# Optimization experiments

Measured on AMD Instinct MI355X. Metric: run time of the kernel, lower is better.

Reference implementation:

```python
import jax, jax.numpy as jnp
import numpy as np

D_MODEL = 2048
D_FFN = 8192
RANK = 16
MOD_SCALE = 0.1
EPS = 1e-6


def setup_inputs() -> dict:
    key = jax.random.key(0)
    ks = jax.random.split(key, 8)
    B, S = 2, 2048
    init_scale = 0.01
    return {
        'hidden_states': jax.random.normal(ks[0], (B, S, D_MODEL), jnp.float32),
        'attn_output': jax.random.normal(ks[1], (B, S, D_MODEL), jnp.float32),
        'A': jax.random.normal(ks[2], (D_MODEL, RANK), jnp.float32) * (init_scale / np.sqrt(D_MODEL)),
        'Bmat': jax.random.normal(ks[3], (RANK, D_FFN), jnp.float32) * (init_scale / np.sqrt(RANK)),
        'W_in': jax.random.normal(ks[4], (D_FFN, D_MODEL), jnp.float32) * 0.02,  # gate_proj.weight
        'W_up': jax.random.normal(ks[5], (D_FFN, D_MODEL), jnp.float32) * 0.02,  # up_proj.weight
        'W_down': jax.random.normal(ks[6], (D_MODEL, D_FFN), jnp.float32) * 0.02,  # down_proj.weight
        'gamma': jnp.ones((D_MODEL,), jnp.float32),  # post_attention_layernorm (RMSNorm) weight
    }


def _rmsnorm(x, gamma):
    var = jnp.mean(x * x, axis=-1, keepdims=True)
    return x * jax.lax.rsqrt(var + EPS) * gamma


def reference(hidden_states, attn_output, A, Bmat, W_in, W_up, W_down, gamma):
    residual = hidden_states
    # Neuro-plastic modulation: [B,S,r]
    modulation = MOD_SCALE * jnp.tanh(jnp.einsum('bsd,dr->bsr', attn_output, A))
    # NPT applies post-attn norm to the residual (not residual+attn)
    h = _rmsnorm(residual, gamma)  # [B,S,d_model]
    # Fused per-token weight delta: delta_w^T @ h == B^T ((A^T h) * mod)
    hA = jnp.einsum('bsd,dr->bsr', h, A)  # [B,S,r]
    delta_out = jnp.einsum('bsr,rf->bsf', hA * modulation, Bmat)  # [B,S,d_ffn]
    gate = jax.nn.silu(jnp.einsum('bsd,fd->bsf', h, W_in) + delta_out)
    up = jnp.einsum('bsd,fd->bsf', h, W_up)
    out = jnp.einsum('bsf,df->bsd', gate * up, W_down)
    return residual + out
```

## Files before the change

kernel.cpp:

```cpp
#include <hip/hip_runtime.h>
#include <cstdint>
#include <cstddef>

#define D_MODEL 2048
#define D_FFN   8192
#define RANK    16
#define EPS     1e-6f
#define MOD_SCALE 0.1f

typedef float    f32x4 __attribute__((ext_vector_type(4)));
typedef _Float16 half8 __attribute__((ext_vector_type(8)));

__device__ __forceinline__ void async_load16(const void* g, void* l) {
  __builtin_amdgcn_global_load_lds(
      (const __attribute__((address_space(1))) uint32_t*)g,
      (__attribute__((address_space(3))) uint32_t*)l,
      16, 0, 0);
}

__device__ __forceinline__ void stage_round(const _Float16* __restrict__ g,
                                            size_t stride, _Float16* l, int tid) {
  const int row = tid >> 3;
  const int cs  = (tid & 7) ^ (row & 7);
  async_load16(g + (size_t)row * stride + (size_t)cs * 8, l + tid * 8);
}

__device__ __forceinline__ half8 frag64(const _Float16* base, int row, int ck) {
  return *(const half8*)&base[row * 64 + ((ck ^ (row & 7)) * 8)];
}

#define PRIO1() __builtin_amdgcn_s_setprio(1)
#define PRIO0() __builtin_amdgcn_s_setprio(0)
#define VMW(n)  asm volatile("s_waitcnt vmcnt(" #n ")" ::: "memory")
#define BARM()  asm volatile("s_barrier" ::: "memory")

__global__ __launch_bounds__(256) void convert3_f32_f16(
    const float* __restrict__ s0, const float* __restrict__ s1,
    const float* __restrict__ s2,
    _Float16* __restrict__ d0, _Float16* __restrict__ d1,
    _Float16* __restrict__ d2)
{
  const int w = blockIdx.x >> 13;
  const float*   s = (w == 0) ? s0 : (w == 1) ? s1 : s2;
  _Float16*      d = (w == 0) ? d0 : (w == 1) ? d1 : d2;
  size_t i = ((size_t)(blockIdx.x & 8191) * 256 + threadIdx.x) * 8;
  f32x4 a = *(const f32x4*)(s + i);
  f32x4 b = *(const f32x4*)(s + i + 4);
  half8 h;
  #pragma unroll
  for (int j = 0; j < 4; ++j) { h[j] = (_Float16)a[j]; h[4+j] = (_Float16)b[j]; }
  *(half8*)(d + i) = h;
}

__global__ __launch_bounds__(256) void convert_f32_f16(
    const float* __restrict__ s, _Float16* __restrict__ d)
{
  size_t i = ((size_t)blockIdx.x * 256 + threadIdx.x) * 8;
  f32x4 a = *(const f32x4*)(s + i);
  f32x4 b = *(const f32x4*)(s + i + 4);
  half8 h;
  #pragma unroll
  for (int j = 0; j < 4; ++j) { h[j] = (_Float16)a[j]; h[4+j] = (_Float16)b[j]; }
  *(half8*)(d + i) = h;
}

__global__ __launch_bounds__(256) void prep_kernel(
    const float* __restrict__ hs, const float* __restrict__ attn,
    const float* __restrict__ Amat, const float* __restrict__ gamma,
    _Float16* __restrict__ h16, float* __restrict__ cmat)
{
  const int token = blockIdx.x;
  const int tid   = threadIdx.x;
  const int lane  = tid & 63;
  const int wv    = tid >> 6;
  const size_t tb = (size_t)token * D_MODEL;
  const int base  = tid * 8;

  f32x4 x0 = *(const f32x4*)(hs + tb + base);
  f32x4 x1 = *(const f32x4*)(hs + tb + base + 4);
  f32x4 a0 = *(const f32x4*)(attn + tb + base);
  f32x4 a1 = *(const f32x4*)(attn + tb + base + 4);

  float ss = 0.f;
  #pragma unroll
  for (int j = 0; j < 4; ++j) ss += x0[j]*x0[j] + x1[j]*x1[j];
  #pragma unroll
  for (int off = 32; off > 0; off >>= 1) ss += __shfl_xor(ss, off, 64);

  __shared__ float red[4];
  __shared__ float redp[4][RANK];
  __shared__ float redh[4][RANK];
  if (lane == 0) red[wv] = ss;
  __syncthreads();
  const float tot = red[0] + red[1] + red[2] + red[3];
  const float rms = rsqrtf(tot * (1.0f / D_MODEL) + EPS);

  f32x4 g0 = *(const f32x4*)(gamma + base);
  f32x4 g1 = *(const f32x4*)(gamma + base + 4);
  float hv[8], av[8];
  #pragma unroll
  for (int j = 0; j < 4; ++j) {
    hv[j]   = x0[j] * rms * g0[j];
    hv[4+j] = x1[j] * rms * g1[j];
    av[j]   = a0[j];
    av[4+j] = a1[j];
  }
  half8 hh;
  #pragma unroll
  for (int j = 0; j < 8; ++j) hh[j] = (_Float16)hv[j];
  *(half8*)(h16 + tb + base) = hh;

  float pa[RANK], ph[RANK];
  #pragma unroll
  for (int r = 0; r < RANK; ++r) { pa[r] = 0.f; ph[r] = 0.f; }
  #pragma unroll
  for (int e = 0; e < 8; ++e) {
    const f32x4* Ar = (const f32x4*)(Amat + (size_t)(base + e) * RANK);
    #pragma unroll
    for (int q = 0; q < 4; ++q) {
      f32x4 ar = Ar[q];
      #pragma unroll
      for (int j = 0; j < 4; ++j) {
        pa[q*4+j] += av[e] * ar[j];
        ph[q*4+j] += hv[e] * ar[j];
      }
    }
  }
  #pragma unroll
  for (int r = 0; r < RANK; ++r) {
    #pragma unroll
    for (int off = 32; off > 0; off >>= 1) {
      pa[r] += __shfl_xor(pa[r], off, 64);
      ph[r] += __shfl_xor(ph[r], off, 64);
    }
  }
  if (lane == 0) {
    #pragma unroll
    for (int r = 0; r < RANK; ++r) { redp[wv][r] = pa[r]; redh[wv][r] = ph[r]; }
  }
  __syncthreads();
  if (tid < RANK) {
    float sp = redp[0][tid] + redp[1][tid] + redp[2][tid] + redp[3][tid];
    float sh = redh[0][tid] + redh[1][tid] + redh[2][tid] + redh[3][tid];
    cmat[(size_t)token * RANK + tid] = sh * (MOD_SCALE * tanhf(sp));
  }
}

#define BGOFF 16384
#define BUOFF 24576

__global__ __launch_bounds__(512, 2) void gemm_gateup(
    const _Float16* __restrict__ h16,
    const _Float16* __restrict__ Wg16, const _Float16* __restrict__ Wu16,
    const float* __restrict__ cmat, const float* __restrict__ Bmat,
    _Float16* __restrict__ tmat)
{
  __shared__ __align__(16) _Float16 lds[2][32768];

  const int tid  = threadIdx.x;
  const int lane = tid & 63;
  const int wv   = tid >> 6;
  const int lr   = lane & 15;
  const int quad = lane >> 4;
  const int qb   = (wv >> 2) * 2;
  const int e    = wv & 3;
  const int wm   = (wv >> 2) * 128;

  const int lin  = blockIdx.x;
  const int xcd  = lin & 7;
  const int r    = lin >> 3;
  const int gm0  = (xcd * 2 + (r & 1)) * 256;
  const int gn0  = (r >> 1) * 128;

  constexpr int NT = D_MODEL / 64;

  f32x4 accG[8][2], accU[8][2];
  #pragma unroll
  for (int i = 0; i < 8; ++i)
    #pragma unroll
    for (int j = 0; j < 2; ++j) {
      f32x4 z = {0.f, 0.f, 0.f, 0.f};
      accG[i][j] = z; accU[i][j] = z;
    }

#define STA(b,q,t)  stage_round(h16  + (size_t)(gm0 + (q)*64) * D_MODEL + (size_t)(t)*64, D_MODEL, &lds[b][(q)*4096], tid)
#define STBG(b,p,t) stage_round(Wg16 + (size_t)(gn0 + (p)*64) * D_MODEL + (size_t)(t)*64, D_MODEL, &lds[b][BGOFF + (p)*4096], tid)
#define STBU(b,p,t) stage_round(Wu16 + (size_t)(gn0 + (p)*64) * D_MODEL + (size_t)(t)*64, D_MODEL, &lds[b][BUOFF + (p)*4096], tid)
#define STAGE_ALL(b,t) do { STA(b,0,t); STA(b,1,t); STA(b,2,t); STA(b,3,t); \
                            STBG(b,0,t); STBG(b,1,t); STBU(b,0,t); STBU(b,1,t); } while (0)

  STAGE_ALL(0, 0);
  VMW(0); BARM();

  for (int t = 0; t < NT; ++t) {
    const int cur = t & 1, nxt = cur ^ 1;
    const _Float16* A   = &lds[cur][0];
    const _Float16* Bgp = &lds[cur][BGOFF + e * 2048];
    const _Float16* Bup = &lds[cur][BUOFF + e * 2048];

    if (t + 1 < NT) STAGE_ALL(nxt, t + 1);

    half8 bg[2][2], bu[2][2], af[4][2];
    #pragma unroll
    for (int inn = 0; inn < 2; ++inn)
      #pragma unroll
      for (int kk = 0; kk < 2; ++kk) {
        bg[inn][kk] = frag64(Bgp, inn*16 + lr, kk*4 + quad);
        bu[inn][kk] = frag64(Bup, inn*16 + lr, kk*4 + quad);
      }
    #pragma unroll
    for (int im = 0; im < 4; ++im)
      #pragma unroll
      for (int kk = 0; kk < 2; ++kk)
        af[im][kk] = frag64(A + (qb + 0) * 4096, im*16 + lr, kk*4 + quad);

    PRIO1();
    #pragma unroll
    for (int im = 0; im < 4; ++im)
      #pragma unroll
      for (int inn = 0; inn < 2; ++inn)
        #pragma unroll
        for (int kk = 0; kk < 2; ++kk) {
          accG[im][inn] = __builtin_amdgcn_mfma_f32_16x16x32_f16(af[im][kk], bg[inn][kk], accG[im][inn], 0, 0, 0);
          accU[im][inn] = __builtin_amdgcn_mfma_f32_16x16x32_f16(af[im][kk], bu[inn][kk], accU[im][inn], 0, 0, 0);
        }
    PRIO0();

    half8 ao[4][2];
    #pragma unroll
    for (int im = 0; im < 4; ++im)
      #pragma unroll
      for (int kk = 0; kk < 2; ++kk)
        ao[im][kk] = frag64(A + (qb + 1) * 4096, im*16 + lr, kk*4 + quad);

    PRIO1();
    #pragma unroll
    for (int im = 0; im < 4; ++im)
      #pragma unroll
      for (int inn = 0; inn < 2; ++inn)
        #pragma unroll
        for (int kk = 0; kk < 2; ++kk) {
          accG[4+im][inn] = __builtin_amdgcn_mfma_f32_16x16x32_f16(ao[im][kk], bg[inn][kk], accG[4+im][inn], 0, 0, 0);
          accU[4+im][inn] = __builtin_amdgcn_mfma_f32_16x16x32_f16(ao[im][kk], bu[inn][kk], accU[4+im][inn], 0, 0, 0);
        }
    PRIO0();

    VMW(0); BARM();
  }

  __syncthreads();
  _Float16* l0 = &lds[0][0];
  for (int i = tid; i < 8192; i += 512) {
    int m = i >> 5, k = i & 31;
    l0[i] = (k < RANK) ? (_Float16)cmat[(size_t)(gm0 + m) * RANK + k] : (_Float16)0.f;
  }
  for (int i = tid; i < 4096; i += 512) {
    int f = i >> 5, k = i & 31;
    l0[8192 + i] = (k < RANK) ? (_Float16)Bmat[(size_t)k * D_FFN + gn0 + f] : (_Float16)0.f;
  }
  __syncthreads();
  #pragma unroll
  for (int ai = 0; ai < 8; ++ai) {
    half8 cf = *(const half8*)&l0[(wm + ai*16 + lr) * 32 + quad * 8];
    #pragma unroll
    for (int inn = 0; inn < 2; ++inn) {
      half8 bd = *(const half8*)&l0[8192 + (e*32 + inn*16 + lr) * 32 + quad * 8];
      accG[ai][inn] = __builtin_amdgcn_mfma_f32_16x16x32_f16(cf, bd, accG[ai][inn], 0, 0, 0);
    }
  }

  #pragma unroll
  for (int ai = 0; ai < 8; ++ai)
    #pragma unroll
    for (int inn = 0; inn < 2; ++inn) {
      const int grow = gm0 + wm + ai*16 + quad*4;
      const int gcol = gn0 + e*32 + inn*16 + lr;
      #pragma unroll
      for (int rr = 0; rr < 4; ++rr) {
        float g = accG[ai][inn][rr];
        float u = accU[ai][inn][rr];
        float s = g / (1.0f + __expf(-g));
        tmat[(size_t)(grow + rr) * D_FFN + gcol] = (_Float16)(s * u);
      }
    }
#undef STA
#undef STBG
#undef STBU
#undef STAGE_ALL
}

__global__ __launch_bounds__(512, 2) void gemm_down(
    const _Float16* __restrict__ tmat, const _Float16* __restrict__ Wd16,
    const float* __restrict__ hs, float* __restrict__ out)
{
  __shared__ __align__(16) _Float16 lds[3][24576];

  const int tid  = threadIdx.x;
  const int lane = tid & 63;
  const int wv   = tid >> 6;
  const int lr   = lane & 15;
  const int quad = lane >> 4;
  const int qb   = (wv >> 2) * 2;
  const int e    = wv & 3;
  const int wm   = (wv >> 2) * 128;

  const int lin  = blockIdx.x;
  const int xcd  = lin & 7;
  const int r    = lin >> 3;
  const int gn0  = (xcd * 2 + (r & 1)) * 128;
  const int gm0  = (r >> 1) * 256;

  constexpr int NT = D_FFN / 64;

  f32x4 acc[8][2];
  #pragma unroll
  for (int i = 0; i < 8; ++i)
    #pragma unroll
    for (int j = 0; j < 2; ++j) {
      f32x4 z = {0.f, 0.f, 0.f, 0.f};
      acc[i][j] = z;
    }

#define DSTA(b,q,t) stage_round(tmat + (size_t)(gm0 + (q)*64) * D_FFN + (size_t)(t)*64, D_FFN, &lds[b][(q)*4096], tid)
#define DSTB(b,p,t) stage_round(Wd16 + (size_t)(gn0 + (p)*64) * D_FFN + (size_t)(t)*64, D_FFN, &lds[b][16384 + (p)*4096], tid)
#define DSTAGE_ALL(b,t) do { DSTA(b,0,t); DSTA(b,1,t); DSTA(b,2,t); DSTA(b,3,t); \
                             DSTB(b,0,t); DSTB(b,1,t); } while (0)

  DSTAGE_ALL(0, 0);
  DSTAGE_ALL(1, 1);
  VMW(6); BARM();

  int cur = 0;
  for (int t = 0; t < NT; ++t) {
    const _Float16* A = &lds[cur][0];
    const _Float16* B = &lds[cur][16384 + e * 2048];
    int nx2 = cur + 2; if (nx2 >= 3) nx2 -= 3;

    if (t + 2 < NT) DSTAGE_ALL(nx2, t + 2);

    half8 bf[2][2], af[4][2];
    #pragma unroll
    for (int inn = 0; inn < 2; ++inn)
      #pragma unroll
      for (int kk = 0; kk < 2; ++kk)
        bf[inn][kk] = frag64(B, inn*16 + lr, kk*4 + quad);
    #pragma unroll
    for (int im = 0; im < 4; ++im)
      #pragma unroll
      for (int kk = 0; kk < 2; ++kk)
        af[im][kk] = frag64(A + (qb + 0) * 4096, im*16 + lr, kk*4 + quad);

    PRIO1();
    #pragma unroll
    for (int im = 0; im < 4; ++im)
      #pragma unroll
      for (int inn = 0; inn < 2; ++inn)
        #pragma unroll
        for (int kk = 0; kk < 2; ++kk)
          acc[im][inn] = __builtin_amdgcn_mfma_f32_16x16x32_f16(af[im][kk], bf[inn][kk], acc[im][inn], 0, 0, 0);
    PRIO0();

    half8 ao[4][2];
    #pragma unroll
    for (int im = 0; im < 4; ++im)
      #pragma unroll
      for (int kk = 0; kk < 2; ++kk)
        ao[im][kk] = frag64(A + (qb + 1) * 4096, im*16 + lr, kk*4 + quad);

    PRIO1();
    #pragma unroll
    for (int im = 0; im < 4; ++im)
      #pragma unroll
      for (int inn = 0; inn < 2; ++inn)
        #pragma unroll
        for (int kk = 0; kk < 2; ++kk)
          acc[4+im][inn] = __builtin_amdgcn_mfma_f32_16x16x32_f16(ao[im][kk], bf[inn][kk], acc[4+im][inn], 0, 0, 0);
    PRIO0();

    if (t + 2 < NT) { VMW(6); } else { VMW(0); }
    BARM();

    cur += 1; if (cur >= 3) cur -= 3;
  }

  #pragma unroll
  for (int ai = 0; ai < 8; ++ai)
    #pragma unroll
    for (int inn = 0; inn < 2; ++inn) {
      const int grow = gm0 + wm + ai*16 + quad*4;
      const int gcol = gn0 + e*32 + inn*16 + lr;
      #pragma unroll
      for (int rr = 0; rr < 4; ++rr) {
        size_t o = (size_t)(grow + rr) * D_MODEL + gcol;
        out[o] = hs[o] + acc[ai][inn][rr];
      }
    }
#undef DSTA
#undef DSTB
#undef DSTAGE_ALL
}

extern "C" void kernel_launch(void* const* d_in, const int* in_sizes, int n_in,
                              void* d_out, int out_size, void* d_ws, size_t ws_size,
                              hipStream_t stream) {
  const float* hs    = (const float*)d_in[0];
  const float* attn  = (const float*)d_in[1];
  const float* Amat  = (const float*)d_in[2];
  const float* Bmat  = (const float*)d_in[3];
  const float* Wg    = (const float*)d_in[4];
  const float* Wu    = (const float*)d_in[5];
  const float* Wd    = (const float*)d_in[6];
  const float* gamma = (const float*)d_in[7];
  float* out = (float*)d_out;

  const int M = in_sizes[0] / D_MODEL;
  const size_t WD = (size_t)D_FFN * D_MODEL;

  char* ws = (char*)d_ws;
  _Float16* h16  = (_Float16*)ws;
  float*    cmat = (float*)(ws + (size_t)M * D_MODEL * 2);
  _Float16* tmat = (_Float16*)(ws + (size_t)M * D_MODEL * 2 + (size_t)M * RANK * 4);
  _Float16* wbuf = tmat + (size_t)M * D_FFN;
  _Float16* Wg16 = wbuf;
  _Float16* Wu16 = wbuf + WD;

  const size_t base_bytes = (size_t)M * D_MODEL * 2 + (size_t)M * RANK * 4
                          + (size_t)M * D_FFN * 2 + 2 * WD * 2;
  const bool sep_wd = (ws_size >= base_bytes + WD * 2);
  _Float16* Wd16 = sep_wd ? (wbuf + 2 * WD) : wbuf;

  const int convBlocks = (int)(WD / (256 * 8));

  prep_kernel<<<M, 256, 0, stream>>>(hs, attn, Amat, gamma, h16, cmat);
  if (sep_wd) {
    convert3_f32_f16<<<3 * convBlocks, 256, 0, stream>>>(Wg, Wu, Wd, Wg16, Wu16, Wd16);
    gemm_gateup<<<dim3((D_FFN / 128) * (M / 256)), 512, 0, stream>>>(h16, Wg16, Wu16, cmat, Bmat, tmat);
  } else {
    convert_f32_f16<<<convBlocks, 256, 0, stream>>>(Wg, Wg16);
    convert_f32_f16<<<convBlocks, 256, 0, stream>>>(Wu, Wu16);
    gemm_gateup<<<dim3((D_FFN / 128) * (M / 256)), 512, 0, stream>>>(h16, Wg16, Wu16, cmat, Bmat, tmat);
    convert_f32_f16<<<convBlocks, 256, 0, stream>>>(Wd, Wd16);
  }
  gemm_down<<<dim3((D_MODEL / 128) * (M / 256)), 512, 0, stream>>>(tmat, Wd16, hs, out);
}
```

Baseline: 734.7 us.

## Restructure gate/up GEMM mainloop into four-phase interleaved load/MFMA schedule

Replaces the simple double-buffered gate/up GEMM loop with a manually unrolled two-tile loop. Each tile is split into four MFMA clusters, with the global-to-LDS staging for the next tile spread between them and barriers plus setprio around each cluster. The goal is to overlap memory traffic with matrix-core work more finely and keep vmcnt waits partial instead of draining fully every iteration. It adds many barriers and tight buffer-reuse ordering (A halves are restaged into a buffer still being read), which risks stalls or races if the wait counts are wrong.

```diff
diff --git a/kernel.cpp b/kernel.cpp
--- a/kernel.cpp
+++ b/kernel.cpp
@@ -32,6 +32,7 @@
 #define PRIO1() __builtin_amdgcn_s_setprio(1)
 #define PRIO0() __builtin_amdgcn_s_setprio(0)
 #define VMW(n)  asm volatile("s_waitcnt vmcnt(" #n ")" ::: "memory")
+#define LKW(n)  asm volatile("s_waitcnt lgkmcnt(" #n ")" ::: "memory")
 #define BARM()  asm volatile("s_barrier" ::: "memory")
 
 __global__ __launch_bounds__(256) void convert3_f32_f16(
@@ -146,6 +147,35 @@
   }
 }
 
+__device__ __forceinline__ void rdA(half8 (&d)[4][2], const _Float16* Ab,
+                                    int lr, int quad) {
+  #pragma unroll
+  for (int im = 0; im < 4; ++im)
+    #pragma unroll
+    for (int kk = 0; kk < 2; ++kk)
+      d[im][kk] = frag64(Ab, im*16 + lr, kk*4 + quad);
+}
+__device__ __forceinline__ void rdB(half8 (&d)[2][2], const _Float16* Bb,
+                                    int lr, int quad) {
+  #pragma unroll
+  for (int inn = 0; inn < 2; ++inn)
+    #pragma unroll
+    for (int kk = 0; kk < 2; ++kk)
+      d[inn][kk] = frag64(Bb, inn*16 + lr, kk*4 + quad);
+}
+__device__ __forceinline__ void cluster(f32x4 (&acc)[8][2], int base,
+                                        const half8 (&a)[4][2],
+                                        const half8 (&b)[2][2]) {
+  #pragma unroll
+  for (int im = 0; im < 4; ++im)
+    #pragma unroll
+    for (int inn = 0; inn < 2; ++inn)
+      #pragma unroll
+      for (int kk = 0; kk < 2; ++kk)
+        acc[base+im][inn] = __builtin_amdgcn_mfma_f32_16x16x32_f16(
+            a[im][kk], b[inn][kk], acc[base+im][inn], 0, 0, 0);
+}
+
 #define BGOFF 16384
 #define BUOFF 24576
 
@@ -172,8 +202,6 @@
   const int gm0  = (xcd * 2 + (r & 1)) * 256;
   const int gn0  = (r >> 1) * 128;
 
-  constexpr int NT = D_MODEL / 64;
-
   f32x4 accG[8][2], accU[8][2];
   #pragma unroll
   for (int i = 0; i < 8; ++i)
@@ -183,69 +211,60 @@
       accG[i][j] = z; accU[i][j] = z;
     }
 
-#define STA(b,q,t)  stage_round(h16  + (size_t)(gm0 + (q)*64) * D_MODEL + (size_t)(t)*64, D_MODEL, &lds[b][(q)*4096], tid)
-#define STBG(b,p,t) stage_round(Wg16 + (size_t)(gn0 + (p)*64) * D_MODEL + (size_t)(t)*64, D_MODEL, &lds[b][BGOFF + (p)*4096], tid)
-#define STBU(b,p,t) stage_round(Wu16 + (size_t)(gn0 + (p)*64) * D_MODEL + (size_t)(t)*64, D_MODEL, &lds[b][BUOFF + (p)*4096], tid)
-#define STAGE_ALL(b,t) do { STA(b,0,t); STA(b,1,t); STA(b,2,t); STA(b,3,t); \
-                            STBG(b,0,t); STBG(b,1,t); STBU(b,0,t); STBU(b,1,t); } while (0)
-
-  STAGE_ALL(0, 0);
-  VMW(0); BARM();
-
-  for (int t = 0; t < NT; ++t) {
-    const int cur = t & 1, nxt = cur ^ 1;
-    const _Float16* A   = &lds[cur][0];
-    const _Float16* Bgp = &lds[cur][BGOFF + e * 2048];
-    const _Float16* Bup = &lds[cur][BUOFF + e * 2048];
-
-    if (t + 1 < NT) STAGE_ALL(nxt, t + 1);
-
-    half8 bg[2][2], bu[2][2], af[4][2];
-    #pragma unroll
-    for (int inn = 0; inn < 2; ++inn)
-      #pragma unroll
-      for (int kk = 0; kk < 2; ++kk) {
-        bg[inn][kk] = frag64(Bgp, inn*16 + lr, kk*4 + quad);
-        bu[inn][kk] = frag64(Bup, inn*16 + lr, kk*4 + quad);
-      }
-    #pragma unroll
-    for (int im = 0; im < 4; ++im)
-      #pragma unroll
-      for (int kk = 0; kk < 2; ++kk)
-        af[im][kk] = frag64(A + (qb + 0) * 4096, im*16 + lr, kk*4 + quad);
-
-    PRIO1();
-    #pragma unroll
-    for (int im = 0; im < 4; ++im)
-      #pragma unroll
-      for (int inn = 0; inn < 2; ++inn)
-        #pragma unroll
-        for (int kk = 0; kk < 2; ++kk) {
-          accG[im][inn] = __builtin_amdgcn_mfma_f32_16x16x32_f16(af[im][kk], bg[inn][kk], accG[im][inn], 0, 0, 0);
-          accU[im][inn] = __builtin_amdgcn_mfma_f32_16x16x32_f16(af[im][kk], bu[inn][kk], accU[im][inn], 0, 0, 0);
-        }
-    PRIO0();
-
-    half8 ao[4][2];
-    #pragma unroll
-    for (int im = 0; im < 4; ++im)
-      #pragma unroll
-      for (int kk = 0; kk < 2; ++kk)
-        ao[im][kk] = frag64(A + (qb + 1) * 4096, im*16 + lr, kk*4 + quad);
-
-    PRIO1();
-    #pragma unroll
-    for (int im = 0; im < 4; ++im)
-      #pragma unroll
-      for (int inn = 0; inn < 2; ++inn)
-        #pragma unroll
-        for (int kk = 0; kk < 2; ++kk) {
-          accG[4+im][inn] = __builtin_amdgcn_mfma_f32_16x16x32_f16(ao[im][kk], bg[inn][kk], accG[4+im][inn], 0, 0, 0);
-          accU[4+im][inn] = __builtin_amdgcn_mfma_f32_16x16x32_f16(ao[im][kk], bu[inn][kk], accU[4+im][inn], 0, 0, 0);
-        }
-    PRIO0();
-
-    VMW(0); BARM();
+#define STAE(b,t) do { \
+    stage_round(h16 + (size_t)(gm0 +   0) * D_MODEL + (size_t)(t)*64, D_MODEL, &lds[b][0],     tid); \
+    stage_round(h16 + (size_t)(gm0 + 128) * D_MODEL + (size_t)(t)*64, D_MODEL, &lds[b][8192],  tid); } while (0)
+#define STAO(b,t) do { \
+    stage_round(h16 + (size_t)(gm0 +  64) * D_MODEL + (size_t)(t)*64, D_MODEL, &lds[b][4096],  tid); \
+    stage_round(h16 + (size_t)(gm0 + 192) * D_MODEL + (size_t)(t)*64, D_MODEL, &lds[b][12288], tid); } while (0)
+#define STG(b,t) do { \
+    stage_round(Wg16 + (size_t)(gn0 +  0) * D_MODEL + (size_t)(t)*64, D_MODEL, &lds[b][BGOFF],        tid); \
+    stage_round(Wg16 + (size_t)(gn0 + 64) * D_MODEL + (size_t)(t)*64, D_MODEL, &lds[b][BGOFF + 4096], tid); } while (0)
+#define STU(b,t) do { \
+    stage_round(Wu16 + (size_t)(gn0 +  0) * D_MODEL + (size_t)(t)*64, D_MODEL, &lds[b][BUOFF],        tid); \
+    stage_round(Wu16 + (size_t)(gn0 + 64) * D_MODEL + (size_t)(t)*64, D_MODEL, &lds[b][BUOFF + 4096], tid); } while (0)
+
+#define PH4(BUF, S1, S2, S3, S4, W4)                                       \
+  {                                                                        \
+    const _Float16* A_  = &lds[BUF][0];                                    \
+    const _Float16* Bg_ = &lds[BUF][BGOFF + e * 2048];                     \
+    const _Float16* Bu_ = &lds[BUF][BUOFF + e * 2048];                     \
+    half8 af[4][2], ao[4][2], bg[2][2], bu[2][2];                          \
+    rdA(af, A_ + qb * 4096, lr, quad);                                     \
+    rdB(bg, Bg_, lr, quad);                                                \
+    S1; LKW(8);                                                            \
+    BARM(); PRIO1(); cluster(accG, 0, af, bg); PRIO0(); BARM();            \
+    rdB(bu, Bu_, lr, quad);                                                \
+    S2;                                                                    \
+    BARM(); PRIO1(); cluster(accU, 0, af, bu); PRIO0(); BARM();            \
+    rdA(ao, A_ + (qb + 1) * 4096, lr, quad);                               \
+    S3;                                                                    \
+    BARM(); PRIO1(); cluster(accU, 4, ao, bu); PRIO0(); BARM();            \
+    S4;                                                                    \
+    BARM(); PRIO1(); cluster(accG, 4, ao, bg); PRIO0();                    \
+    W4; BARM();                                                            \
+  }
+
+  STAE(0, 0); STAO(0, 0); STG(0, 0); STU(0, 0);
+  STG(1, 1);  STU(1, 1);  STAE(1, 1);
+  VMW(6); BARM();
+
+  #pragma unroll 1
+  for (int i = 0; i < 16; ++i) {
+    const int t1 = 2*i + 1, t2 = 2*i + 2, t3 = 2*i + 3;
+    const bool more = (i < 15);
+    PH4(0,
+        { STAO(1, t1); },
+        { if (more) STG(0, t2); },
+        { if (more) STU(0, t2); },
+        { if (more) STAE(0, t2); },
+        { if (more) { VMW(6); } else { VMW(0); } });
+    PH4(1,
+        { if (more) STAO(0, t2); },
+        { if (more) STG(1, t3); },
+        { if (more) STU(1, t3); },
+        { if (more) STAE(1, t3); },
+        { if (more) { VMW(6); } else { VMW(0); } });
   }
 
   __syncthreads();
@@ -283,10 +302,11 @@
         tmat[(size_t)(grow + rr) * D_FFN + gcol] = (_Float16)(s * u);
       }
     }
-#undef STA
-#undef STBG
-#undef STBU
-#undef STAGE_ALL
+#undef STAE
+#undef STAO
+#undef STG
+#undef STU
+#undef PH4
 }
 
 __global__ __launch_bounds__(512, 2) void gemm_down(
```

Measured after the change: 743.0 us. About the same (+1.1%).

## Use 4-wave blocks with larger per-wave tiles in both FFN GEMMs

Applied to the files above, without the earlier changes.

Both GEMM kernels now run 256-thread blocks in which each wave computes a 128x64 output tile, doubling per-wave fragment reuse and cutting LDS fragment reads per MFMA. The down-projection also moves from a 3-stage to a 2-stage LDS pipeline with a full wait each iteration. This trades fewer waves per CU, heavy accumulator register pressure and a shallower prefetch depth for better register-level reuse.

```diff
diff --git a/kernel.cpp b/kernel.cpp
--- a/kernel.cpp
+++ b/kernel.cpp
@@ -149,7 +149,7 @@
 #define BGOFF 16384
 #define BUOFF 24576
 
-__global__ __launch_bounds__(512, 2) void gemm_gateup(
+__global__ __launch_bounds__(256, 1) void gemm_gateup(
     const _Float16* __restrict__ h16,
     const _Float16* __restrict__ Wg16, const _Float16* __restrict__ Wu16,
     const float* __restrict__ cmat, const float* __restrict__ Bmat,
@@ -162,9 +162,8 @@
   const int wv   = tid >> 6;
   const int lr   = lane & 15;
   const int quad = lane >> 4;
-  const int qb   = (wv >> 2) * 2;
-  const int e    = wv & 3;
-  const int wm   = (wv >> 2) * 128;
+  const int wm   = (wv >> 1) * 128;
+  const int wn   = (wv & 1) * 64;
 
   const int lin  = blockIdx.x;
   const int xcd  = lin & 7;
@@ -172,77 +171,76 @@
   const int gm0  = (xcd * 2 + (r & 1)) * 256;
   const int gn0  = (r >> 1) * 128;
 
-  constexpr int NT = D_MODEL / 64;
-
-  f32x4 accG[8][2], accU[8][2];
+  f32x4 accG[8][4], accU[8][4];
   #pragma unroll
   for (int i = 0; i < 8; ++i)
     #pragma unroll
-    for (int j = 0; j < 2; ++j) {
+    for (int j = 0; j < 4; ++j) {
       f32x4 z = {0.f, 0.f, 0.f, 0.f};
       accG[i][j] = z; accU[i][j] = z;
     }
 
-#define STA(b,q,t)  stage_round(h16  + (size_t)(gm0 + (q)*64) * D_MODEL + (size_t)(t)*64, D_MODEL, &lds[b][(q)*4096], tid)
-#define STBG(b,p,t) stage_round(Wg16 + (size_t)(gn0 + (p)*64) * D_MODEL + (size_t)(t)*64, D_MODEL, &lds[b][BGOFF + (p)*4096], tid)
-#define STBU(b,p,t) stage_round(Wu16 + (size_t)(gn0 + (p)*64) * D_MODEL + (size_t)(t)*64, D_MODEL, &lds[b][BUOFF + (p)*4096], tid)
-#define STAGE_ALL(b,t) do { STA(b,0,t); STA(b,1,t); STA(b,2,t); STA(b,3,t); \
-                            STBG(b,0,t); STBG(b,1,t); STBU(b,0,t); STBU(b,1,t); } while (0)
+#define STAGE_ALL(b,t) do {                                                          \
+    _Pragma("unroll")                                                                \
+    for (int j = 0; j < 8; ++j)                                                      \
+      stage_round(h16  + (size_t)(gm0 + j*32) * D_MODEL + (size_t)(t)*64, D_MODEL,   \
+                  &lds[b][j*2048], tid);                                             \
+    _Pragma("unroll")                                                                \
+    for (int j = 0; j < 4; ++j)                                                      \
+      stage_round(Wg16 + (size_t)(gn0 + j*32) * D_MODEL + (size_t)(t)*64, D_MODEL,   \
+                  &lds[b][BGOFF + j*2048], tid);                                     \
+    _Pragma("unroll")                                                                \
+    for (int j = 0; j < 4; ++j)                                                      \
+      stage_round(Wu16 + (size_t)(gn0 + j*32) * D_MODEL + (size_t)(t)*64, D_MODEL,   \
+                  &lds[b][BUOFF + j*2048], tid);                                     \
+  } while (0)
 
   STAGE_ALL(0, 0);
   VMW(0); BARM();
 
+  constexpr int NT = D_MODEL / 64;
   for (int t = 0; t < NT; ++t) {
     const int cur = t & 1, nxt = cur ^ 1;
-    const _Float16* A   = &lds[cur][0];
-    const _Float16* Bgp = &lds[cur][BGOFF + e * 2048];
-    const _Float16* Bup = &lds[cur][BUOFF + e * 2048];
-
     if (t + 1 < NT) STAGE_ALL(nxt, t + 1);
 
-    half8 bg[2][2], bu[2][2], af[4][2];
-    #pragma unroll
-    for (int inn = 0; inn < 2; ++inn)
-      #pragma unroll
-      for (int kk = 0; kk < 2; ++kk) {
-        bg[inn][kk] = frag64(Bgp, inn*16 + lr, kk*4 + quad);
-        bu[inn][kk] = frag64(Bup, inn*16 + lr, kk*4 + quad);
+    const _Float16* A_  = &lds[cur][wm * 64];
+    const _Float16* Bg_ = &lds[cur][BGOFF + wn * 64];
+    const _Float16* Bu_ = &lds[cur][BUOFF + wn * 64];
+
+    half8 a0[8], a1[8], bg[4], bu[4];
+    #pragma unroll
+    for (int im = 0; im < 8; ++im) a0[im] = frag64(A_, im*16 + lr, quad);
+    #pragma unroll
+    for (int inn = 0; inn < 4; ++inn) {
+      bg[inn] = frag64(Bg_, inn*16 + lr, quad);
+      bu[inn] = frag64(Bu_, inn*16 + lr, quad);
+    }
+    #pragma unroll
+    for (int im = 0; im < 8; ++im) a1[im] = frag64(A_, im*16 + lr, 4 + quad);
+
+    PRIO1();
+    #pragma unroll
+    for (int im = 0; im < 8; ++im)
+      #pragma unroll
+      for (int inn = 0; inn < 4; ++inn) {
+        accG[im][inn] = __builtin_amdgcn_mfma_f32_16x16x32_f16(a0[im], bg[inn], accG[im][inn], 0, 0, 0);
+        accU[im][inn] = __builtin_amdgcn_mfma_f32_16x16x32_f16(a0[im], bu[inn], accU[im][inn], 0, 0, 0);
       }
-    #pragma unroll
-    for (int im = 0; im < 4; ++im)
-      #pragma unroll
-      for (int kk = 0; kk < 2; ++kk)
-        af[im][kk] = frag64(A + (qb + 0) * 4096, im*16 + lr, kk*4 + quad);
-
+    PRIO0();
+
+    #pragma unroll
+    for (int inn = 0; inn < 4; ++inn) {
+      bg[inn] = frag64(Bg_, inn*16 + lr, 4 + quad);
+      bu[inn] = frag64(Bu_, inn*16 + lr, 4 + quad);
+    }
     PRIO1();
     #pragma unroll
-    for (int im = 0; im < 4; ++im)
-      #pragma unroll
-      for (int inn = 0; inn < 2; ++inn)
-        #pragma unroll
-        for (int kk = 0; kk < 2; ++kk) {
-          accG[im][inn] = __builtin_amdgcn_mfma_f32_16x16x32_f16(af[im][kk], bg[inn][kk], accG[im][inn], 0, 0, 0);
-          accU[im][inn] = __builtin_amdgcn_mfma_f32_16x16x32_f16(af[im][kk], bu[inn][kk], accU[im][inn], 0, 0, 0);
-        }
-    PRIO0();
-
-    half8 ao[4][2];
-    #pragma unroll
-    for (int im = 0; im < 4; ++im)
-      #pragma unroll
-      for (int kk = 0; kk < 2; ++kk)
-        ao[im][kk] = frag64(A + (qb + 1) * 4096, im*16 + lr, kk*4 + quad);
-
-    PRIO1();
-    #pragma unroll
-    for (int im = 0; im < 4; ++im)
-      #pragma unroll
-      for (int inn = 0; inn < 2; ++inn)
-        #pragma unroll
-        for (int kk = 0; kk < 2; ++kk) {
-          accG[4+im][inn] = __builtin_amdgcn_mfma_f32_16x16x32_f16(ao[im][kk], bg[inn][kk], accG[4+im][inn], 0, 0, 0);
-          accU[4+im][inn] = __builtin_amdgcn_mfma_f32_16x16x32_f16(ao[im][kk], bu[inn][kk], accU[4+im][inn], 0, 0, 0);
-        }
+    for (int im = 0; im < 8; ++im)
+      #pragma unroll
+      for (int inn = 0; inn < 4; ++inn) {
+        accG[im][inn] = __builtin_amdgcn_mfma_f32_16x16x32_f16(a1[im], bg[inn], accG[im][inn], 0, 0, 0);
+        accU[im][inn] = __builtin_amdgcn_mfma_f32_16x16x32_f16(a1[im], bu[inn], accU[im][inn], 0, 0, 0);
+      }
     PRIO0();
 
     VMW(0); BARM();
@@ -250,11 +248,11 @@
 
   __syncthreads();
   _Float16* l0 = &lds[0][0];
-  for (int i = tid; i < 8192; i += 512) {
+  for (int i = tid; i < 8192; i += 256) {
     int m = i >> 5, k = i & 31;
     l0[i] = (k < RANK) ? (_Float16)cmat[(size_t)(gm0 + m) * RANK + k] : (_Float16)0.f;
   }
-  for (int i = tid; i < 4096; i += 512) {
+  for (int i = tid; i < 4096; i += 256) {
     int f = i >> 5, k = i & 31;
     l0[8192 + i] = (k < RANK) ? (_Float16)Bmat[(size_t)k * D_FFN + gn0 + f] : (_Float16)0.f;
   }
@@ -263,8 +261,8 @@
   for (int ai = 0; ai < 8; ++ai) {
     half8 cf = *(const half8*)&l0[(wm + ai*16 + lr) * 32 + quad * 8];
     #pragma unroll
-    for (int inn = 0; inn < 2; ++inn) {
-      half8 bd = *(const half8*)&l0[8192 + (e*32 + inn*16 + lr) * 32 + quad * 8];
+    for (int inn = 0; inn < 4; ++inn) {
+      half8 bd = *(const half8*)&l0[8192 + (wn + inn*16 + lr) * 32 + quad * 8];
       accG[ai][inn] = __builtin_amdgcn_mfma_f32_16x16x32_f16(cf, bd, accG[ai][inn], 0, 0, 0);
     }
   }
@@ -272,9 +270,9 @@
   #pragma unroll
   for (int ai = 0; ai < 8; ++ai)
     #pragma unroll
-    for (int inn = 0; inn < 2; ++inn) {
+    for (int inn = 0; inn < 4; ++inn) {
       const int grow = gm0 + wm + ai*16 + quad*4;
-      const int gcol = gn0 + e*32 + inn*16 + lr;
+      const int gcol = gn0 + wn + inn*16 + lr;
       #pragma unroll
       for (int rr = 0; rr < 4; ++rr) {
         float g = accG[ai][inn][rr];
@@ -283,26 +281,22 @@
         tmat[(size_t)(grow + rr) * D_FFN + gcol] = (_Float16)(s * u);
       }
     }
-#undef STA
-#undef STBG
-#undef STBU
 #undef STAGE_ALL
 }
 
-__global__ __launch_bounds__(512, 2) void gemm_down(
+__global__ __launch_bounds__(256, 1) void gemm_down(
     const _Float16* __restrict__ tmat, const _Float16* __restrict__ Wd16,
     const float* __restrict__ hs, float* __restrict__ out)
 {
-  __shared__ __align__(16) _Float16 lds[3][24576];
+  __shared__ __align__(16) _Float16 lds[2][24576];
 
   const int tid  = threadIdx.x;
   const int lane = tid & 63;
   const int wv   = tid >> 6;
   const int lr   = lane & 15;
   const int quad = lane >> 4;
-  const int qb   = (wv >> 2) * 2;
-  const int e    = wv & 3;
-  const int wm   = (wv >> 2) * 128;
+  const int wm   = (wv >> 1) * 128;
+  const int wn   = (wv & 1) * 64;
 
   const int lin  = blockIdx.x;
   const int xcd  = lin & 7;
@@ -312,91 +306,77 @@
 
   constexpr int NT = D_FFN / 64;
 
-  f32x4 acc[8][2];
+  f32x4 acc[8][4];
   #pragma unroll
   for (int i = 0; i < 8; ++i)
     #pragma unroll
-    for (int j = 0; j < 2; ++j) {
+    for (int j = 0; j < 4; ++j) {
       f32x4 z = {0.f, 0.f, 0.f, 0.f};
       acc[i][j] = z;
     }
 
-#define DSTA(b,q,t) stage_round(tmat + (size_t)(gm0 + (q)*64) * D_FFN + (size_t)(t)*64, D_FFN, &lds[b][(q)*4096], tid)
-#define DSTB(b,p,t) stage_round(Wd16 + (size_t)(gn0 + (p)*64) * D_FFN + (size_t)(t)*64, D_FFN, &lds[b][16384 + (p)*4096], tid)
-#define DSTAGE_ALL(b,t) do { DSTA(b,0,t); DSTA(b,1,t); DSTA(b,2,t); DSTA(b,3,t); \
-                             DSTB(b,0,t); DSTB(b,1,t); } while (0)
+#define DSTAGE_ALL(b,t) do {                                                         \
+    _Pragma("unroll")                                                                \
+    for (int j = 0; j < 8; ++j)                                                      \
+      stage_round(tmat + (size_t)(gm0 + j*32) * D_FFN + (size_t)(t)*64, D_FFN,       \
+                  &lds[b][j*2048], tid);                                             \
+    _Pragma("unroll")                                                                \
+    for (int j = 0; j < 4; ++j)                                                      \
+      stage_round(Wd16 + (size_t)(gn0 + j*32) * D_FFN + (size_t)(t)*64, D_FFN,       \
+                  &lds[b][16384 + j*2048], tid);                                     \
+  } while (0)
 
   DSTAGE_ALL(0, 0);
-  DSTAGE_ALL(1, 1);
-  VMW(6); BARM();
-
-  int cur = 0;
+  VMW(0); BARM();
+
   for (int t = 0; t < NT; ++t) {
-    const _Float16* A = &lds[cur][0];
-    const _Float16* B = &lds[cur][16384 + e * 2048];
-    int nx2 = cur + 2; if (nx2 >= 3) nx2 -= 3;
-
-    if (t + 2 < NT) DSTAGE_ALL(nx2, t + 2);
-
-    half8 bf[2][2], af[4][2];
-    #pragma unroll
-    for (int inn = 0; inn < 2; ++inn)
-      #pragma unroll
-      for (int kk = 0; kk < 2; ++kk)
-        bf[inn][kk] = frag64(B, inn*16 + lr, kk*4 + quad);
-    #pragma unroll
-    for (int im = 0; im < 4; ++im)
-      #pragma unroll
-      for (int kk = 0; kk < 2; ++kk)
-        af[im][kk] = frag64(A + (qb + 0) * 4096, im*16 + lr, kk*4 + quad);
+    const int cur = t & 1, nxt = cur ^ 1;
+    if (t + 1 < NT) DSTAGE_ALL(nxt, t + 1);
+
+    const _Float16* A_ = &lds[cur][wm * 64];
+    const _Float16* B_ = &lds[cur][16384 + wn * 64];
+
+    half8 a0[8], a1[8], b0[4];
+    #pragma unroll
+    for (int im = 0; im < 8; ++im) a0[im] = frag64(A_, im*16 + lr, quad);
+    #pragma unroll
+    for (int inn = 0; inn < 4; ++inn) b0[inn] = frag64(B_, inn*16 + lr, quad);
+    #pragma unroll
+    for (int im = 0; im < 8; ++im) a1[im] = frag64(A_, im*16 + lr, 4 + quad);
 
     PRIO1();
     #pragma unroll
-    for (int im = 0; im < 4; ++im)
-      #pragma unroll
-      for (int inn = 0; inn < 2; ++inn)
-        #pragma unroll
-        for (int kk = 0; kk < 2; ++kk)
-          acc[im][inn] = __builtin_amdgcn_mfma_f32_16x16x32_f16(af[im][kk], bf[inn][kk], acc[im][inn], 0, 0, 0);
+    for (int im = 0; im < 8; ++im)
+      #pragma unroll
+      for (int inn = 0; inn < 4; ++inn)
+        acc[im][inn] = __builtin_amdgcn_mfma_f32_16x16x32_f16(a0[im], b0[inn], acc[im][inn], 0, 0, 0);
     PRIO0();
 
-    half8 ao[4][2];
-    #pragma unroll
-    for (int im = 0; im < 4; ++im)
-      #pragma unroll
-      for (int kk = 0; kk < 2; ++kk)
-        ao[im][kk] = frag64(A + (qb + 1) * 4096, im*16 + lr, kk*4 + quad);
-
+    #pragma unroll
+    for (int inn = 0; inn < 4; ++inn) b0[inn] = frag64(B_, inn*16 + lr, 4 + quad);
     PRIO1();
     #pragma unroll
-    for (int im = 0; im < 4; ++im)
-      #pragma unroll
-      for (int inn = 0; inn < 2; ++inn)
-        #pragma unroll
-        for (int kk = 0; kk < 2; ++kk)
-          acc[4+im][inn] = __builtin_amdgcn_mfma_f32_16x16x32_f16(ao[im][kk], bf[inn][kk], acc[4+im][inn], 0, 0, 0);
+    for (int im = 0; im < 8; ++im)
+      #pragma unroll
+      for (int inn = 0; inn < 4; ++inn)
+        acc[im][inn] = __builtin_amdgcn_mfma_f32_16x16x32_f16(a1[im], b0[inn], acc[im][inn], 0, 0, 0);
     PRIO0();
 
-    if (t + 2 < NT) { VMW(6); } else { VMW(0); }
-    BARM();
-
-    cur += 1; if (cur >= 3) cur -= 3;
+    VMW(0); BARM();
   }
 
   #pragma unroll
   for (int ai = 0; ai < 8; ++ai)
     #pragma unroll
-    for (int inn = 0; inn < 2; ++inn) {
+    for (int inn = 0; inn < 4; ++inn) {
       const int grow = gm0 + wm + ai*16 + quad*4;
-      const int gcol = gn0 + e*32 + inn*16 + lr;
+      const int gcol = gn0 + wn + inn*16 + lr;
       #pragma unroll
       for (int rr = 0; rr < 4; ++rr) {
         size_t o = (size_t)(grow + rr) * D_MODEL + gcol;
         out[o] = hs[o] + acc[ai][inn][rr];
       }
     }
-#undef DSTA
-#undef DSTB
 #undef DSTAGE_ALL
 }
 
@@ -434,12 +414,12 @@
   prep_kernel<<<M, 256, 0, stream>>>(hs, attn, Amat, gamma, h16, cmat);
   if (sep_wd) {
     convert3_f32_f16<<<3 * convBlocks, 256, 0, stream>>>(Wg, Wu, Wd, Wg16, Wu16, Wd16);
-    gemm_gateup<<<dim3((D_FFN / 128) * (M / 256)), 512, 0, stream>>>(h16, Wg16, Wu16, cmat, Bmat, tmat);
+    gemm_gateup<<<dim3((D_FFN / 128) * (M / 256)), 256, 0, stream>>>(h16, Wg16, Wu16, cmat, Bmat, tmat);
   } else {
     convert_f32_f16<<<convBlocks, 256, 0, stream>>>(Wg, Wg16);
     convert_f32_f16<<<convBlocks, 256, 0, stream>>>(Wu, Wu16);
-    gemm_gateup<<<dim3((D_FFN / 128) * (M / 256)), 512, 0, stream>>>(h16, Wg16, Wu16, cmat, Bmat, tmat);
+    gemm_gateup<<<dim3((D_FFN / 128) * (M / 256)), 256, 0, stream>>>(h16, Wg16, Wu16, cmat, Bmat, tmat);
     convert_f32_f16<<<convBlocks, 256, 0, stream>>>(Wd, Wd16);
   }
-  gemm_down<<<dim3((D_MODEL / 128) * (M / 256)), 512, 0, stream>>>(tmat, Wd16, hs, out);
-}
+  gemm_down<<<dim3((D_MODEL / 128) * (M / 256)), 256, 0, stream>>>(tmat, Wd16, hs, out);
+}
```

Result: slower. 830.1 us (+13.0%).
